# Kernel optimization log

Hardware: AMD Instinct MI355X
Metric: run time of the kernel (lower is better)

Reference implementation:

```python
import jax, jax.numpy as jnp
import numpy as np

H = 1024
NH = 16
DH = H // NH

def setup_inputs() -> dict:
    key = jax.random.key(0)
    ks = jax.random.split(key, 6)
    s = 1.0 / np.sqrt(H)
    x = jax.random.normal(ks[0], (4, 2048, H), dtype=jnp.float32)
    Wq = jax.random.uniform(ks[1], (H, H), jnp.float32, -s, s)
    Wk = jax.random.uniform(ks[2], (H, H), jnp.float32, -s, s)
    Wv = jax.random.uniform(ks[3], (H, H), jnp.float32, -s, s)
    Wo = jax.random.uniform(ks[4], (H, H), jnp.float32, -s, s)
    bo = jax.random.uniform(ks[5], (H,), jnp.float32, -s, s)
    return {"x": x, "Wq": Wq, "Wk": Wk, "Wv": Wv, "Wo": Wo, "bo": bo}

def reference(x, Wq, Wk, Wv, Wo, bo):
    B, T, Hd = x.shape
    # projections: torch Linear is x @ W.T
    def split_heads(y):
        return y.reshape(B, T, NH, DH).transpose(0, 2, 1, 3)  # [B, nh, T, dh]
    Q = split_heads(x @ Wq.T)
    K = split_heads(x @ Wk.T)
    V = split_heads(x @ Wv.T)
    scores = jnp.einsum('bhtd,bhsd->bhts', Q, K) / jnp.sqrt(jnp.float32(DH))
    w = jax.nn.softmax(scores, axis=-1)
    ctx = jnp.einsum('bhts,bhsd->bhtd', w, V)  # [B, nh, T, dh]
    ctx = ctx.transpose(0, 2, 1, 3).reshape(B, T, Hd)
    out = ctx @ Wo.T + bo  # [B, T, H]
    return out.mean(axis=1)  # [B, H]
```

## Files before the change

### kernel.cpp

```cpp
#include <hip/hip_runtime.h>
#include <hip/hip_bf16.h>
#include <cstdint>

#define BB   4
#define TT   2048
#define HH   1024
#define NHH  16
#define DHH  64
#define MM   (BB*TT)

typedef __attribute__((ext_vector_type(8))) short short8;
typedef __attribute__((ext_vector_type(4))) short short4v;
typedef __attribute__((ext_vector_type(4))) float f32x4;

#if __has_builtin(__builtin_amdgcn_exp2f)
#define EXP2F(x) __builtin_amdgcn_exp2f(x)
#else
#define EXP2F(x) exp2f(x)
#endif

#define QSCALE 0.1803368801111204f

__device__ __forceinline__ float bf2f(unsigned short u) {
    return __uint_as_float(((uint32_t)u) << 16);
}
__device__ __forceinline__ unsigned short f2bf(float f) {
    uint32_t u = __float_as_uint(f);
    return (unsigned short)((u + 0x7fffu + ((u >> 16) & 1u)) >> 16);
}
__device__ __forceinline__ void gload_lds16(const unsigned short* g, unsigned short* l) {
    __builtin_amdgcn_global_load_lds(
        (const __attribute__((address_space(1))) uint32_t*)g,
        (__attribute__((address_space(3))) uint32_t*)l, 16, 0, 0);
}

__device__ __forceinline__ f32x4 mfma16(short4v a, short4v b, f32x4 c) {
#if __has_builtin(__builtin_amdgcn_mfma_f32_16x16x16bf16_1k)
    return __builtin_amdgcn_mfma_f32_16x16x16bf16_1k(a, b, c, 0, 0, 0);
#else
    f32x4 d;
    asm("v_mfma_f32_16x16x16_bf16 %0, %1, %2, %3"
        : "=v"(d) : "v"(a), "v"(b), "v"(c));
    return d;
#endif
}

__global__ __launch_bounds__(256) void cvt_bf16(
    const float* __restrict__ src, unsigned short* __restrict__ dst, int n4)
{
    int i = blockIdx.x * 256 + threadIdx.x;
    const int stride = gridDim.x * 256;
    for (; i < n4; i += stride) {
        float4 v = ((const float4*)src)[i];
        ushort4 o;
        o.x = f2bf(v.x); o.y = f2bf(v.y); o.z = f2bf(v.z); o.w = f2bf(v.w);
        ((ushort4*)dst)[i] = o;
    }
}

__global__ __launch_bounds__(256) void cvt_w3(
    const float* __restrict__ Wq, const float* __restrict__ Wk,
    const float* __restrict__ Wv, unsigned short* __restrict__ Wb)
{
    const float* src = (blockIdx.y == 0) ? Wq : (blockIdx.y == 1 ? Wk : Wv);
    unsigned short* dst = Wb + (size_t)blockIdx.y * HH * HH;
    const int n4 = HH * HH / 4;
    int i = blockIdx.x * 256 + threadIdx.x;
    const int stride = gridDim.x * 256;
    for (; i < n4; i += stride) {
        float4 v = ((const float4*)src)[i];
        ushort4 o;
        o.x = f2bf(v.x); o.y = f2bf(v.y); o.z = f2bf(v.z); o.w = f2bf(v.w);
        ((ushort4*)dst)[i] = o;
    }
}

__global__ __launch_bounds__(256) void proj_mfma(
    const unsigned short* __restrict__ xb, const unsigned short* __restrict__ Wb,
    unsigned short* __restrict__ qp, unsigned short* __restrict__ kp,
    unsigned short* __restrict__ vp)
{
    __shared__ unsigned short As[4096];
    __shared__ unsigned short Bs[4096];
    const int m0 = blockIdx.x * 128;
    const int n0 = blockIdx.y * 128;
    const int sel = n0 >> 10;
    const unsigned short* Wbase = Wb + (size_t)sel * HH * HH;
    const int nw0 = n0 & (HH - 1);
    const int tid = threadIdx.x;
    const int wave = tid >> 6, lane = tid & 63;
    const int quad = lane >> 4, l15 = lane & 15;
    const int wm = wave >> 1, wn = wave & 1;

    f32x4 acc[4][4];
    #pragma unroll
    for (int i = 0; i < 4; ++i)
        #pragma unroll
        for (int j = 0; j < 4; ++j) acc[i][j] = (f32x4){0.f, 0.f, 0.f, 0.f};

    for (int k0 = 0; k0 < HH; k0 += 32) {
        __syncthreads();
        #pragma unroll
        for (int q = 0; q < 2; ++q) {
            const int chunk = (wave * 2 + q) * 64 + lane;
            const int kc = chunk >> 7, mrow = chunk & 127;
            gload_lds16(xb    + (size_t)(m0  + mrow) * HH + k0 + kc * 8, As + chunk * 8);
            gload_lds16(Wbase + (size_t)(nw0 + mrow) * HH + k0 + kc * 8, Bs + chunk * 8);
        }
        __syncthreads();
        short8 af[4], bf[4];
        #pragma unroll
        for (int i = 0; i < 4; ++i)
            af[i] = *(const short8*)&As[(quad * 128 + wm * 64 + i * 16 + l15) * 8];
        #pragma unroll
        for (int j = 0; j < 4; ++j)
            bf[j] = *(const short8*)&Bs[(quad * 128 + wn * 64 + j * 16 + l15) * 8];
        #pragma unroll
        for (int i = 0; i < 4; ++i)
            #pragma unroll
            for (int j = 0; j < 4; ++j)
                acc[i][j] = __builtin_amdgcn_mfma_f32_16x16x32_bf16(af[i], bf[j], acc[i][j], 0, 0, 0);
    }

    unsigned short* outp = (sel == 0) ? qp : (sel == 1 ? kp : vp);
    const float cscale = (sel == 0) ? QSCALE : 1.0f;

    unsigned short* eb = As;
    const int lr_st = tid >> 3;
    const int k8    = tid & 7;
    const int row_g = m0 + ((lr_st & 16) ? 64 : 0) + (lr_st & 15);
    #pragma unroll
    for (int i = 0; i < 4; ++i) {
        __syncthreads();
        #pragma unroll
        for (int j = 0; j < 4; ++j) {
            const int c = wn * 64 + j * 16 + l15;
            #pragma unroll
            for (int r = 0; r < 4; ++r)
                eb[(wm * 16 + quad * 4 + r) * 128 + c] = f2bf(acc[i][j][r] * cscale);
        }
        __syncthreads();
        if (sel < 2) {
            const int row = row_g + i * 16;
            const int bb2 = row >> 11, tt2 = row & (TT - 1);
            {
                const int col = n0 + k8 * 8;
                const int hh2 = (col >> 6) & (NHH - 1);
                *(short8*)(&outp[((size_t)(bb2 * NHH + hh2) * TT + tt2) * DHH + (col & 63)]) =
                    *(const short8*)(&eb[lr_st * 128 + k8 * 8]);
            }
            {
                const int col = n0 + 64 + k8 * 8;
                const int hh2 = (col >> 6) & (NHH - 1);
                *(short8*)(&outp[((size_t)(bb2 * NHH + hh2) * TT + tt2) * DHH + (col & 63)]) =
                    *(const short8*)(&eb[lr_st * 128 + 64 + k8 * 8]);
            }
        } else {
            const int c = tid & 127;
            const int rn = tid >> 7;
            const int colg = nw0 + c;
            const int hh2 = (colg >> 6) & (NHH - 1);
            const int dd = colg & 63;
            #pragma unroll
            for (int rr = 0; rr < 2; ++rr) {
                const int run = rn + rr * 2;
                const int tb = m0 + ((run >= 2) ? 64 : 0) + i * 16 + (run & 1) * 8;
                const int bb2 = tb >> 11, tt2 = tb & (TT - 1);
                short8 v;
                #pragma unroll
                for (int j = 0; j < 8; ++j)
                    v[j] = (short)eb[(run * 8 + j) * 128 + c];
                *(short8*)(&outp[((size_t)(bb2 * NHH + hh2) * DHH + dd) * TT + tt2]) = v;
            }
        }
    }
}

__global__ __launch_bounds__(256) void attn_flash(
    const unsigned short* __restrict__ qp, const unsigned short* __restrict__ kp,
    const unsigned short* __restrict__ vt, float* __restrict__ cm)
{
    const int h = blockIdx.x, b = blockIdx.z;
    const int bh = b * NHH + h;
    const int tid = threadIdx.x;
    const int wave = tid >> 6, lane = tid & 63;
    const int quad = lane >> 4, l15 = lane & 15;
    const int t0w = blockIdx.y * 128 + wave * 32;

    __shared__ unsigned short lK[2048];
    __shared__ unsigned short lV[2048];

    const unsigned short* q  = qp + (size_t)bh * TT * DHH;
    const unsigned short* kg = kp + (size_t)bh * TT * DHH;
    const unsigned short* vg = vt + (size_t)bh * DHH * TT;

    const int krow = tid >> 3, kc8 = (tid & 7) ^ (krow & 7);
    const int vrow = tid >> 2, vc4 = (tid & 3) ^ (vrow & 3);

    short8 aq[2][2];
    #pragma unroll
    for (int g = 0; g < 2; ++g)
        #pragma unroll
        for (int c = 0; c < 2; ++c)
            aq[g][c] = *(const short8*)&q[(size_t)(t0w + g * 16 + l15) * DHH + quad * 8 + c * 32];

    const f32x4 zk = {0.f, 0.f, 0.f, 0.f};
    f32x4 acc[2][4];
    #pragma unroll
    for (int g = 0; g < 2; ++g)
        #pragma unroll
        for (int dc = 0; dc < 4; ++dc) acc[g][dc] = zk;
    float den0 = 0.f, den1 = 0.f;

#define MAKE_P(sreg, den, preg)                                              \
    {                                                                        \
        float e0 = EXP2F(sreg[0]), e1 = EXP2F(sreg[1]);                      \
        float e2 = EXP2F(sreg[2]), e3 = EXP2F(sreg[3]);                      \
        den += (e0 + e1) + (e2 + e3);                                        \
        preg[0] = (short)f2bf(e0); preg[1] = (short)f2bf(e1);                \
        preg[2] = (short)f2bf(e2); preg[3] = (short)f2bf(e3);                \
    }

    for (int ss = 0; ss < 64; ++ss) {
        const int s0 = ss * 32;
        __syncthreads();
        gload_lds16(kg + (size_t)(s0 + krow) * DHH + kc8 * 8, lK + tid * 8);
        gload_lds16(vg + (size_t)vrow * TT + s0 + vc4 * 8,    lV + tid * 8);
        __syncthreads();

        short8 kf[2][2];
        #pragma unroll
        for (int st = 0; st < 2; ++st) {
            const int row = st * 16 + l15;
            kf[st][0] = *(const short8*)&lK[row * 64 + ((quad)     ^ (row & 7)) * 8];
            kf[st][1] = *(const short8*)&lK[row * 64 + ((4 + quad) ^ (row & 7)) * 8];
        }
        short4v vf[4][2];
        #pragma unroll
        for (int dc = 0; dc < 4; ++dc) {
            const int d = dc * 16 + l15;
            #pragma unroll
            for (int st = 0; st < 2; ++st) {
                const int ch = (st * 2 + (quad >> 1)) ^ (d & 3);
                vf[dc][st] = *(const short4v*)&lV[d * 32 + ch * 8 + (quad & 1) * 4];
            }
        }

        f32x4 s00 = __builtin_amdgcn_mfma_f32_16x16x32_bf16(kf[0][0], aq[0][0], zk, 0, 0, 0);
        s00 = __builtin_amdgcn_mfma_f32_16x16x32_bf16(kf[0][1], aq[0][1], s00, 0, 0, 0);
        f32x4 s01 = __builtin_amdgcn_mfma_f32_16x16x32_bf16(kf[1][0], aq[0][0], zk, 0, 0, 0);
        s01 = __builtin_amdgcn_mfma_f32_16x16x32_bf16(kf[1][1], aq[0][1], s01, 0, 0, 0);
        f32x4 s10 = __builtin_amdgcn_mfma_f32_16x16x32_bf16(kf[0][0], aq[1][0], zk, 0, 0, 0);
        s10 = __builtin_amdgcn_mfma_f32_16x16x32_bf16(kf[0][1], aq[1][1], s10, 0, 0, 0);
        f32x4 s11 = __builtin_amdgcn_mfma_f32_16x16x32_bf16(kf[1][0], aq[1][0], zk, 0, 0, 0);
        s11 = __builtin_amdgcn_mfma_f32_16x16x32_bf16(kf[1][1], aq[1][1], s11, 0, 0, 0);

        short4v p00, p01, p10, p11;
        MAKE_P(s00, den0, p00);
        MAKE_P(s01, den0, p01);
        MAKE_P(s10, den1, p10);
        MAKE_P(s11, den1, p11);

        #pragma unroll
        for (int dc = 0; dc < 4; ++dc) {
            acc[0][dc] = mfma16(vf[dc][0], p00, acc[0][dc]);
            acc[0][dc] = mfma16(vf[dc][1], p01, acc[0][dc]);
            acc[1][dc] = mfma16(vf[dc][0], p10, acc[1][dc]);
            acc[1][dc] = mfma16(vf[dc][1], p11, acc[1][dc]);
        }
    }
#undef MAKE_P

    den0 += __shfl_xor(den0, 16); den0 += __shfl_xor(den0, 32);
    den1 += __shfl_xor(den1, 16); den1 += __shfl_xor(den1, 32);
    const float inv0 = 1.0f / (den0 * (float)TT);
    const float inv1 = 1.0f / (den1 * (float)TT);

    #pragma unroll
    for (int dc = 0; dc < 4; ++dc) {
        #pragma unroll
        for (int r = 0; r < 4; ++r) {
            float v = acc[0][dc][r] * inv0 + acc[1][dc][r] * inv1;
            v += __shfl_xor(v, 1); v += __shfl_xor(v, 2);
            v += __shfl_xor(v, 4); v += __shfl_xor(v, 8);
            if (l15 == 0)
                atomicAdd(&cm[b * HH + h * DHH + dc * 16 + quad * 4 + r], v);
        }
    }
}

__global__ __launch_bounds__(256) void out_proj(
    const float* __restrict__ cm, const float* __restrict__ Wo,
    const float* __restrict__ bo, float* __restrict__ out)
{
    const int b = blockIdx.y;
    const int jb = blockIdx.x;
    const int tid = threadIdx.x;
    const int j = jb * 64 + (tid >> 2);
    const int kg = tid & 3;
    __shared__ float cs[HH];
    for (int k = tid; k < HH; k += 256) cs[k] = cm[b * HH + k];
    __syncthreads();
    float acc = 0.f;
    const float* wrow = &Wo[(size_t)j * HH];
    #pragma unroll 8
    for (int i = 0; i < 64; ++i) {
        const int k = kg * 256 + i * 4;
        float4 w4 = *(const float4*)&wrow[k];
        acc += w4.x * cs[k] + w4.y * cs[k+1] + w4.z * cs[k+2] + w4.w * cs[k+3];
    }
    acc += __shfl_down(acc, 2, 4);
    acc += __shfl_down(acc, 1, 4);
    if (kg == 0) out[b * HH + j] = acc + bo[j];
}

extern "C" void kernel_launch(void* const* d_in, const int* in_sizes, int n_in,
                              void* d_out, int out_size, void* d_ws, size_t ws_size,
                              hipStream_t stream) {
    const float* x  = (const float*)d_in[0];
    const float* Wq = (const float*)d_in[1];
    const float* Wk = (const float*)d_in[2];
    const float* Wv = (const float*)d_in[3];
    const float* Wo = (const float*)d_in[4];
    const float* bo = (const float*)d_in[5];
    float* out = (float*)d_out;

    char* ws = (char*)d_ws;
    unsigned short* qp = (unsigned short*)ws;  ws += (size_t)MM * HH * 2;
    unsigned short* kp = (unsigned short*)ws;  ws += (size_t)MM * HH * 2;
    unsigned short* vt = (unsigned short*)ws;  ws += (size_t)MM * HH * 2;
    unsigned short* xb = (unsigned short*)ws;  ws += (size_t)MM * HH * 2;
    unsigned short* Wb = (unsigned short*)ws;  ws += (size_t)3 * HH * HH * 2;
    float* cm = (float*)ws;

    hipMemsetAsync(cm, 0, (size_t)BB * HH * 4, stream);

    cvt_bf16<<<2048, 256, 0, stream>>>(x, xb, MM * HH / 4);
    cvt_w3  <<<dim3(512, 3), 256, 0, stream>>>(Wq, Wk, Wv, Wb);

    proj_mfma <<<dim3(64, 24),      256, 0, stream>>>(xb, Wb, qp, kp, vt);
    attn_flash<<<dim3(NHH, 16, BB), 256, 0, stream>>>(qp, kp, vt, cm);
    out_proj  <<<dim3(16, BB),      256, 0, stream>>>(cm, Wo, bo, out);
}
```

Measured before the change: 323.7 us.

## Store V in MFMA-fragment order and load it directly from global, skipping LDS

The projection kernel now writes V in a tiled layout matching the MFMA B-fragment order, so the attention kernel loads V fragments straight from global memory into registers instead of staging them through LDS. Each wave now handles 16 query rows instead of 32, and the grid doubles in the query dimension to keep total work the same. This removes the LDS traffic and bank-conflict swizzling for V and raises parallelism. In exchange, K/V reuse per block is halved, so global/L2 traffic for K and V doubles, and the direct global loads may add latency inside the loop.

```diff
diff --git a/kernel.cpp b/kernel.cpp
--- a/kernel.cpp
+++ b/kernel.cpp
@@ -170,7 +170,10 @@
                 #pragma unroll
                 for (int j = 0; j < 8; ++j)
                     v[j] = (short)eb[(run * 8 + j) * 128 + c];
-                *(short8*)(&outp[((size_t)(bb2 * NHH + hh2) * DHH + dd) * TT + tt2]) = v;
+                const size_t off = (size_t)(bb2 * NHH + hh2) * (TT * DHH)
+                    + (tt2 >> 5) * 2048 + (dd >> 4) * 512 + ((tt2 >> 4) & 1) * 256
+                    + (dd & 15) * 16 + ((tt2 >> 2) & 3) * 4;
+                *(short8*)(&outp[off]) = v;
             }
         }
     }
@@ -185,34 +188,28 @@
     const int tid = threadIdx.x;
     const int wave = tid >> 6, lane = tid & 63;
     const int quad = lane >> 4, l15 = lane & 15;
-    const int t0w = blockIdx.y * 128 + wave * 32;
+    const int t0 = blockIdx.y * 64 + wave * 16;
 
     __shared__ unsigned short lK[2048];
-    __shared__ unsigned short lV[2048];
 
     const unsigned short* q  = qp + (size_t)bh * TT * DHH;
     const unsigned short* kg = kp + (size_t)bh * TT * DHH;
-    const unsigned short* vg = vt + (size_t)bh * DHH * TT;
+    const unsigned short* vb = vt + (size_t)bh * TT * DHH + l15 * 16 + quad * 4;
 
     const int krow = tid >> 3, kc8 = (tid & 7) ^ (krow & 7);
-    const int vrow = tid >> 2, vc4 = (tid & 3) ^ (vrow & 3);
-
-    short8 aq[2][2];
-    #pragma unroll
-    for (int g = 0; g < 2; ++g)
-        #pragma unroll
-        for (int c = 0; c < 2; ++c)
-            aq[g][c] = *(const short8*)&q[(size_t)(t0w + g * 16 + l15) * DHH + quad * 8 + c * 32];
+
+    short8 aq[2];
+    #pragma unroll
+    for (int c = 0; c < 2; ++c)
+        aq[c] = *(const short8*)&q[(size_t)(t0 + l15) * DHH + quad * 8 + c * 32];
 
     const f32x4 zk = {0.f, 0.f, 0.f, 0.f};
-    f32x4 acc[2][4];
-    #pragma unroll
-    for (int g = 0; g < 2; ++g)
-        #pragma unroll
-        for (int dc = 0; dc < 4; ++dc) acc[g][dc] = zk;
-    float den0 = 0.f, den1 = 0.f;
-
-#define MAKE_P(sreg, den, preg)                                              \
+    f32x4 acc[4];
+    #pragma unroll
+    for (int dc = 0; dc < 4; ++dc) acc[dc] = zk;
+    float den = 0.f;
+
+#define MAKE_P(sreg, preg)                                                   \
     {                                                                        \
         float e0 = EXP2F(sreg[0]), e1 = EXP2F(sreg[1]);                      \
         float e2 = EXP2F(sreg[2]), e3 = EXP2F(sreg[3]);                      \
@@ -225,7 +222,13 @@
         const int s0 = ss * 32;
         __syncthreads();
         gload_lds16(kg + (size_t)(s0 + krow) * DHH + kc8 * 8, lK + tid * 8);
-        gload_lds16(vg + (size_t)vrow * TT + s0 + vc4 * 8,    lV + tid * 8);
+        short4v vf[4][2];
+        const unsigned short* vbs = vb + ss * 2048;
+        #pragma unroll
+        for (int dc = 0; dc < 4; ++dc)
+            #pragma unroll
+            for (int st = 0; st < 2; ++st)
+                vf[dc][st] = *(const short4v*)(vbs + dc * 512 + st * 256);
         __syncthreads();
 
         short8 kf[2][2];
@@ -235,52 +238,33 @@
             kf[st][0] = *(const short8*)&lK[row * 64 + ((quad)     ^ (row & 7)) * 8];
             kf[st][1] = *(const short8*)&lK[row * 64 + ((4 + quad) ^ (row & 7)) * 8];
         }
-        short4v vf[4][2];
+
+        f32x4 sf0 = __builtin_amdgcn_mfma_f32_16x16x32_bf16(kf[0][0], aq[0], zk, 0, 0, 0);
+        sf0 = __builtin_amdgcn_mfma_f32_16x16x32_bf16(kf[0][1], aq[1], sf0, 0, 0, 0);
+        f32x4 sf1 = __builtin_amdgcn_mfma_f32_16x16x32_bf16(kf[1][0], aq[0], zk, 0, 0, 0);
+        sf1 = __builtin_amdgcn_mfma_f32_16x16x32_bf16(kf[1][1], aq[1], sf1, 0, 0, 0);
+
+        short4v p0, p1;
+        MAKE_P(sf0, p0);
+        MAKE_P(sf1, p1);
+
         #pragma unroll
         for (int dc = 0; dc < 4; ++dc) {
-            const int d = dc * 16 + l15;
-            #pragma unroll
-            for (int st = 0; st < 2; ++st) {
-                const int ch = (st * 2 + (quad >> 1)) ^ (d & 3);
-                vf[dc][st] = *(const short4v*)&lV[d * 32 + ch * 8 + (quad & 1) * 4];
-            }
-        }
-
-        f32x4 s00 = __builtin_amdgcn_mfma_f32_16x16x32_bf16(kf[0][0], aq[0][0], zk, 0, 0, 0);
-        s00 = __builtin_amdgcn_mfma_f32_16x16x32_bf16(kf[0][1], aq[0][1], s00, 0, 0, 0);
-        f32x4 s01 = __builtin_amdgcn_mfma_f32_16x16x32_bf16(kf[1][0], aq[0][0], zk, 0, 0, 0);
-        s01 = __builtin_amdgcn_mfma_f32_16x16x32_bf16(kf[1][1], aq[0][1], s01, 0, 0, 0);
-        f32x4 s10 = __builtin_amdgcn_mfma_f32_16x16x32_bf16(kf[0][0], aq[1][0], zk, 0, 0, 0);
-        s10 = __builtin_amdgcn_mfma_f32_16x16x32_bf16(kf[0][1], aq[1][1], s10, 0, 0, 0);
-        f32x4 s11 = __builtin_amdgcn_mfma_f32_16x16x32_bf16(kf[1][0], aq[1][0], zk, 0, 0, 0);
-        s11 = __builtin_amdgcn_mfma_f32_16x16x32_bf16(kf[1][1], aq[1][1], s11, 0, 0, 0);
-
-        short4v p00, p01, p10, p11;
-        MAKE_P(s00, den0, p00);
-        MAKE_P(s01, den0, p01);
-        MAKE_P(s10, den1, p10);
-        MAKE_P(s11, den1, p11);
-
-        #pragma unroll
-        for (int dc = 0; dc < 4; ++dc) {
-            acc[0][dc] = mfma16(vf[dc][0], p00, acc[0][dc]);
-            acc[0][dc] = mfma16(vf[dc][1], p01, acc[0][dc]);
-            acc[1][dc] = mfma16(vf[dc][0], p10, acc[1][dc]);
-            acc[1][dc] = mfma16(vf[dc][1], p11, acc[1][dc]);
+            acc[dc] = mfma16(vf[dc][0], p0, acc[dc]);
+            acc[dc] = mfma16(vf[dc][1], p1, acc[dc]);
         }
     }
 #undef MAKE_P
 
-    den0 += __shfl_xor(den0, 16); den0 += __shfl_xor(den0, 32);
-    den1 += __shfl_xor(den1, 16); den1 += __shfl_xor(den1, 32);
-    const float inv0 = 1.0f / (den0 * (float)TT);
-    const float inv1 = 1.0f / (den1 * (float)TT);
+    den += __shfl_xor(den, 16);
+    den += __shfl_xor(den, 32);
+    const float inv = 1.0f / (den * (float)TT);
 
     #pragma unroll
     for (int dc = 0; dc < 4; ++dc) {
         #pragma unroll
         for (int r = 0; r < 4; ++r) {
-            float v = acc[0][dc][r] * inv0 + acc[1][dc][r] * inv1;
+            float v = acc[dc][r] * inv;
             v += __shfl_xor(v, 1); v += __shfl_xor(v, 2);
             v += __shfl_xor(v, 4); v += __shfl_xor(v, 8);
             if (l15 == 0)
@@ -339,6 +323,6 @@
     cvt_w3  <<<dim3(512, 3), 256, 0, stream>>>(Wq, Wk, Wv, Wb);
 
     proj_mfma <<<dim3(64, 24),      256, 0, stream>>>(xb, Wb, qp, kp, vt);
-    attn_flash<<<dim3(NHH, 16, BB), 256, 0, stream>>>(qp, kp, vt, cm);
+    attn_flash<<<dim3(NHH, 32, BB), 256, 0, stream>>>(qp, kp, vt, cm);
     out_proj  <<<dim3(16, BB),      256, 0, stream>>>(cm, Wo, bo, out);
 }
```

Result: slower. 375.6 us (+16.0%).
